# Optimization experiments

Measured on AMD Instinct MI355X. Metric: run time of the kernel, lower is better.

Reference implementation:

```python
import jax, jax.numpy as jnp
import numpy as np

OUTCOMES = [8, 8, 8, 8, 8, 8]           # concept outcome counts (concepts_order)
N_TOTAL = int(np.prod(OUTCOMES))        # 262144 joint states
N_VALID = 8192                          # admissible states
B, D = 4096, 1024


def setup_inputs() -> dict:
    key = jax.random.key(0)
    k1, k2 = jax.random.split(key)
    embeddings = jax.random.normal(k1, (B, D), dtype=jnp.float32)
    W = jax.random.normal(k2, (N_VALID, D), dtype=jnp.float32) * 0.02
    b = jnp.zeros((N_VALID,), dtype=jnp.float32)
    # unique sorted admissible-state indices, like torch.argwhere(mask)
    rng = np.random.default_rng(0)
    valid_states = jnp.asarray(
        np.sort(rng.choice(N_TOTAL, size=N_VALID, replace=False)).astype(np.int32))
    return {"embeddings": embeddings, "W": W, "b": b, "valid_states": valid_states}


def reference(embeddings, W, b, valid_states):
    # softmax over valid states: [B, N_VALID]
    probs = jax.nn.softmax(embeddings @ W.T + b, axis=1)
    probs_t = probs.T  # [N_VALID, B] for leading-axis segment reduction
    marginals = []
    stride = N_TOTAL
    for n_i in OUTCOMES:
        stride //= n_i
        # digit of each valid joint-state index along this concept's axis
        digit = (valid_states // stride) % n_i  # [N_VALID]
        # equivalent to scattering probs into the full joint tensor and
        # summing over all other concept axes, without materializing it
        m = jax.ops.segment_sum(probs_t, digit, num_segments=n_i).T  # [B, n_i]
        marginals.append(m)
    return jnp.stack(marginals)  # [n_concepts, B, 8]
```

## Files before the change

kernel.cpp:

```cpp
#include <hip/hip_runtime.h>
#include <hip/hip_bf16.h>
#include <cstdint>
#include <cstddef>

typedef __bf16 bf16_t;
typedef bf16_t bf16x8 __attribute__((ext_vector_type(8)));
typedef bf16_t bf16x4 __attribute__((ext_vector_type(4)));
typedef float  f32x4  __attribute__((ext_vector_type(4)));
typedef float  f32x16 __attribute__((ext_vector_type(16)));
typedef unsigned int u32;

#define BROWS 4096
#define NV    8192
#define KD    1024
#define NT    16
#define ST    48
#define LOG2E 1.44269504088896340736f

#define GLL(gsrc, ldst) \
  __builtin_amdgcn_global_load_lds((const __attribute__((address_space(1))) u32*)(gsrc), \
                                   (__attribute__((address_space(3))) u32*)(ldst), 16, 0, 0)
#define FENCE asm volatile("" ::: "memory")

__global__ void prep_kernel(const float* __restrict__ E, const float* __restrict__ W,
                            const int* __restrict__ vs,
                            bf16_t* __restrict__ Eb, bf16_t* __restrict__ Wb,
                            bf16_t* __restrict__ s2t) {
  const int nE = BROWS * KD / 4;
  const int nW = NV * KD / 4;
  const int nS = ST * NV / 8;
  const int nT = nE + nW + nS;
  int idx = blockIdx.x * blockDim.x + threadIdx.x;
  int stride = gridDim.x * blockDim.x;
  for (int i = idx; i < nT; i += stride) {
    if (i < nE + nW) {
      const float4* s; bf16x4* d; int j;
      if (i < nE) { s = (const float4*)E; d = (bf16x4*)Eb; j = i; }
      else        { s = (const float4*)W; d = (bf16x4*)Wb; j = i - nE; }
      float4 v = s[j];
      bf16x4 o;
      o[0] = (bf16_t)v.x; o[1] = (bf16_t)v.y; o[2] = (bf16_t)v.z; o[3] = (bf16_t)v.w;
      d[j] = o;
    } else {
      int u  = i - nE - nW;
      int b  = u >> 10;
      int i0 = (u & 1023) * 8;
      int c = b >> 3, d = b & 7, sh = 15 - 3 * c;
      bf16x8 o;
#pragma unroll
      for (int e = 0; e < 8; ++e)
        o[e] = (bf16_t)((((vs[i0 + e] >> sh) & 7) == d) ? 1.0f : 0.0f);
      *(bf16x8*)(s2t + (size_t)b * NV + i0) = o;
    }
  }
}

__global__ __launch_bounds__(512, 2)
void gemm_fused_kernel(const bf16_t* __restrict__ W, const bf16_t* __restrict__ E,
                       const float* __restrict__ bias, const bf16_t* __restrict__ s2t,
                       float* __restrict__ part) {
  __shared__ __align__(16) char lds[2][65536];
  #define AKH0 0
  #define AKH1 16384
  #define BKH0 32768
  #define BKH1 49152
  #define SOFF 75776

  const int t    = threadIdx.x;
  const int lane = t & 63;
  const int wv   = t >> 6;
  const int wm   = wv >> 2;
  const int wn   = wv & 3;
  const int fr   = lane & 15;
  const int fq   = lane >> 4;
  const int l31  = lane & 31;
  const int hi   = lane >> 5;

  int bid = blockIdx.x;
  int wg  = (bid & 7) * 64 + (bid >> 3);
  const int stile = wg >> 4;
  const int btile = wg & 15;
  const int st0 = stile * 256;
  const int bt0 = btile * 256;

  const int srow = lane >> 2;
  const int skel = ((lane & 3) ^ ((lane >> 3) & 3)) * 8;
  const bf16_t* aptr = W + (size_t)(st0 + wv * 32 + srow) * KD + skel;
  const bf16_t* bptr = E + (size_t)(bt0 + wv * 32 + srow) * KD + skel;
  const int dchunk = (wv * 2) * 1024;

  const int inner  = (hi * 16) ^ ((l31 & 6) << 3);
  const int a_base = wm * 8192 + l31 * 64 + inner;
  const int b_base = wn * 4096 + l31 * 64 + inner;

  f32x16 acc[4][2] = {};

  GLL(aptr,                &lds[0][AKH0 + dchunk]);
  GLL(aptr + 16 * KD,      &lds[0][AKH0 + dchunk + 1024]);
  GLL(bptr,                &lds[0][BKH0 + dchunk]);
  GLL(bptr + 16 * KD,      &lds[0][BKH0 + dchunk + 1024]);
  GLL(aptr + 32,           &lds[0][AKH1 + dchunk]);
  GLL(aptr + 32 + 16 * KD, &lds[0][AKH1 + dchunk + 1024]);
  GLL(bptr + 32,           &lds[0][BKH1 + dchunk]);
  GLL(bptr + 32 + 16 * KD, &lds[0][BKH1 + dchunk + 1024]);
  asm volatile("s_waitcnt vmcnt(0)" ::: "memory");
  __builtin_amdgcn_s_barrier();
  FENCE;

  int cur = 0;
  for (int kt = 0; kt < NT; ++kt) {
    const char* bufp = lds[cur];
    char* nbuf = lds[cur ^ 1];
    const bool pf = (kt + 1 < NT);

    bf16x8 a0[4][2], b0[2][2], a1[4][2], b1[2][2];

#pragma unroll
    for (int n = 0; n < 2; ++n)
#pragma unroll
      for (int ks = 0; ks < 2; ++ks)
        b0[n][ks] = *(const bf16x8*)(bufp + BKH0 + (b_base ^ (ks << 5)) + n * 2048);
#pragma unroll
    for (int m = 0; m < 4; ++m)
#pragma unroll
      for (int ks = 0; ks < 2; ++ks)
        a0[m][ks] = *(const bf16x8*)(bufp + AKH0 + (a_base ^ (ks << 5)) + m * 2048);

    if (pf) {
      const bf16_t* an = aptr + (kt + 1) * 64;
      const bf16_t* bn = bptr + (kt + 1) * 64;
      GLL(an,                &nbuf[AKH0 + dchunk]);
      GLL(an + 16 * KD,      &nbuf[AKH0 + dchunk + 1024]);
      GLL(bn,                &nbuf[BKH0 + dchunk]);
      GLL(bn + 16 * KD,      &nbuf[BKH0 + dchunk + 1024]);
      GLL(an + 32,           &nbuf[AKH1 + dchunk]);
      GLL(an + 32 + 16 * KD, &nbuf[AKH1 + dchunk + 1024]);
      GLL(bn + 32,           &nbuf[BKH1 + dchunk]);
      GLL(bn + 32 + 16 * KD, &nbuf[BKH1 + dchunk + 1024]);
    }

#pragma unroll
    for (int n = 0; n < 2; ++n)
#pragma unroll
      for (int ks = 0; ks < 2; ++ks)
        b1[n][ks] = *(const bf16x8*)(bufp + BKH1 + (b_base ^ (ks << 5)) + n * 2048);
#pragma unroll
    for (int m = 0; m < 4; ++m)
#pragma unroll
      for (int ks = 0; ks < 2; ++ks)
        a1[m][ks] = *(const bf16x8*)(bufp + AKH1 + (a_base ^ (ks << 5)) + m * 2048);

    __builtin_amdgcn_s_setprio(1);
#pragma unroll
    for (int ks = 0; ks < 2; ++ks)
#pragma unroll
      for (int m = 0; m < 4; ++m)
#pragma unroll
        for (int n = 0; n < 2; ++n)
          acc[m][n] = __builtin_amdgcn_mfma_f32_32x32x16_bf16(a0[m][ks], b0[n][ks], acc[m][n], 0, 0, 0);
#pragma unroll
    for (int ks = 0; ks < 2; ++ks)
#pragma unroll
      for (int m = 0; m < 4; ++m)
#pragma unroll
        for (int n = 0; n < 2; ++n)
          acc[m][n] = __builtin_amdgcn_mfma_f32_32x32x16_bf16(a1[m][ks], b1[n][ks], acc[m][n], 0, 0, 0);
    __builtin_amdgcn_s_setprio(0);

    asm volatile("s_waitcnt vmcnt(0)" ::: "memory");
    __builtin_amdgcn_sched_barrier(0);
    __builtin_amdgcn_s_barrier();
    FENCE;
    cur ^= 1;
  }

  char* const ldsf = &lds[0][0];

  bf16x8 sreg[3];
#pragma unroll
  for (int q = 0; q < 3; ++q) {
    const int c = t * 3 + q;
    sreg[q] = *(const bf16x8*)(s2t + (size_t)(c >> 5) * NV + st0 + (c & 31) * 8);
  }

  float* const ppart = part + (size_t)bt0 * (32 * ST) + (size_t)stile * ST;

#pragma unroll
  for (int pass = 0; pass < 2; ++pass) {
    if ((wn >> 1) == pass) {
      const int j = (wn & 1) * 64 + l31;
#pragma unroll
      for (int m = 0; m < 4; ++m)
#pragma unroll
        for (int n = 0; n < 2; ++n)
#pragma unroll
          for (int g = 0; g < 4; ++g) {
            const float4 bb = *(const float4*)&bias[st0 + wm * 128 + m * 32 + g * 8 + hi * 4];
            bf16x4 ev;
            ev[0] = (bf16_t)exp2f((acc[m][n][g * 4 + 0] + bb.x) * LOG2E);
            ev[1] = (bf16_t)exp2f((acc[m][n][g * 4 + 1] + bb.y) * LOG2E);
            ev[2] = (bf16_t)exp2f((acc[m][n][g * 4 + 2] + bb.z) * LOG2E);
            ev[3] = (bf16_t)exp2f((acc[m][n][g * 4 + 3] + bb.w) * LOG2E);
            *(bf16x4*)(ldsf + (j + n * 32) * 592 + wm * 256 + m * 64 + g * 16 + hi * 8) = ev;
          }
    }
    if (pass == 0) {
#pragma unroll
      for (int q = 0; q < 3; ++q) {
        const int c = t * 3 + q;
        *(bf16x8*)(ldsf + SOFF + (c >> 5) * 592 + (c & 31) * 16) = sreg[q];
      }
    }
    __syncthreads();

    f32x4 acc2[3] = {{0.f,0.f,0.f,0.f},{0.f,0.f,0.f,0.f},{0.f,0.f,0.f,0.f}};
#pragma unroll
    for (int k2 = 0; k2 < 8; ++k2) {
      const bf16x8 ea = *(const bf16x8*)(ldsf + (wv * 16 + fr) * 592 + k2 * 64 + fq * 16);
#pragma unroll
      for (int n2 = 0; n2 < 3; ++n2) {
        const bf16x8 sb = *(const bf16x8*)(ldsf + SOFF + (n2 * 16 + fr) * 592 + k2 * 64 + fq * 16);
        acc2[n2] = __builtin_amdgcn_mfma_f32_16x16x32_bf16(ea, sb, acc2[n2], 0, 0, 0);
      }
    }
    const int jg = pass * 128 + wv * 16 + fq * 4;
#pragma unroll
    for (int n2 = 0; n2 < 3; ++n2)
#pragma unroll
      for (int r = 0; r < 4; ++r)
        ppart[(size_t)(jg + r) * (32 * ST) + n2 * 16 + fr] = acc2[n2][r];
    __syncthreads();
  }
}

__global__ __launch_bounds__(64)
void reduce_kernel(const float* __restrict__ part, float* __restrict__ out) {
  const int b = blockIdx.x;
  const int t = threadIdx.x;
  __shared__ float fin[ST];
  if (t < ST) {
    const float* p = part + (size_t)b * (32 * ST) + t;
    float s = 0.f;
#pragma unroll
    for (int mt = 0; mt < 32; ++mt)
      s += p[mt * ST];
    fin[t] = s;
  }
  __syncthreads();
  if (t < ST) {
    float total = fin[0] + fin[1] + fin[2] + fin[3] + fin[4] + fin[5] + fin[6] + fin[7];
    out[(size_t)(t >> 3) * BROWS * 8 + (size_t)b * 8 + (t & 7)] = fin[t] / total;
  }
}

extern "C" void kernel_launch(void* const* d_in, const int* in_sizes, int n_in,
                              void* d_out, int out_size, void* d_ws, size_t ws_size,
                              hipStream_t stream) {
  const float* E    = (const float*)d_in[0];
  const float* W    = (const float*)d_in[1];
  const float* bias = (const float*)d_in[2];
  const int*   vs   = (const int*)d_in[3];
  float* out = (float*)d_out;

  char* ws = (char*)d_ws;
  size_t off = 0;
  bf16_t* Eb   = (bf16_t*)(ws + off); off += (size_t)BROWS * KD * 2;
  bf16_t* Wb   = (bf16_t*)(ws + off); off += (size_t)NV * KD * 2;
  bf16_t* s2t  = (bf16_t*)(ws + off); off += (size_t)ST * NV * 2;
  float*  part = (float*)(ws + off);  off += (size_t)BROWS * 32 * ST * 4;

  prep_kernel<<<3072, 256, 0, stream>>>(E, W, vs, Eb, Wb, s2t);
  gemm_fused_kernel<<<512, 512, 0, stream>>>(Wb, Eb, bias, s2t, part);
  reduce_kernel<<<BROWS, 64, 0, stream>>>(part, out);
}
```

Measured before the change: 109.1 us.

## Switch main GEMM to 16x16x32 MFMA tiles with XOR-swizzled LDS epilogue

Replaces the 32x32x16 MFMA accumulation with 16x16x32 MFMAs over an 8x4 accumulator grid and rewrites the LDS read addressing and swizzle to match. The epilogue now stores exp values in an XOR-swizzled 512-byte row layout instead of padded 592-byte rows. The indicator matrix is loaded straight into LDS with global_load_lds, using a pre-swizzled layout produced in the prep kernel. The aims are fewer LDS bank conflicts, no register staging for the indicator tiles, and a possibly better MFMA issue pattern. The cost is more MFMA instructions per k-step, since each one covers a smaller tile.

```diff
diff --git a/kernel.cpp b/kernel.cpp
--- a/kernel.cpp
+++ b/kernel.cpp
@@ -7,7 +7,6 @@
 typedef bf16_t bf16x8 __attribute__((ext_vector_type(8)));
 typedef bf16_t bf16x4 __attribute__((ext_vector_type(4)));
 typedef float  f32x4  __attribute__((ext_vector_type(4)));
-typedef float  f32x16 __attribute__((ext_vector_type(16)));
 typedef unsigned int u32;
 
 #define BROWS 4096
@@ -45,11 +44,12 @@
       int u  = i - nE - nW;
       int b  = u >> 10;
       int i0 = (u & 1023) * 8;
+      int base = i0 ^ ((b & 7) << 3);
       int c = b >> 3, d = b & 7, sh = 15 - 3 * c;
       bf16x8 o;
 #pragma unroll
       for (int e = 0; e < 8; ++e)
-        o[e] = (bf16_t)((((vs[i0 + e] >> sh) & 7) == d) ? 1.0f : 0.0f);
+        o[e] = (bf16_t)((((vs[base + e] >> sh) & 7) == d) ? 1.0f : 0.0f);
       *(bf16x8*)(s2t + (size_t)b * NV + i0) = o;
     }
   }
@@ -64,7 +64,6 @@
   #define AKH1 16384
   #define BKH0 32768
   #define BKH1 49152
-  #define SOFF 75776
 
   const int t    = threadIdx.x;
   const int lane = t & 63;
@@ -73,8 +72,6 @@
   const int wn   = wv & 3;
   const int fr   = lane & 15;
   const int fq   = lane >> 4;
-  const int l31  = lane & 31;
-  const int hi   = lane >> 5;
 
   int bid = blockIdx.x;
   int wg  = (bid & 7) * 64 + (bid >> 3);
@@ -89,11 +86,11 @@
   const bf16_t* bptr = E + (size_t)(bt0 + wv * 32 + srow) * KD + skel;
   const int dchunk = (wv * 2) * 1024;
 
-  const int inner  = (hi * 16) ^ ((l31 & 6) << 3);
-  const int a_base = wm * 8192 + l31 * 64 + inner;
-  const int b_base = wn * 4096 + l31 * 64 + inner;
-
-  f32x16 acc[4][2] = {};
+  const int xsw    = (fr & 6) << 3;
+  const int a_base = wm * 8192 + ((fr * 64 + fq * 16) ^ xsw);
+  const int b_base = wn * 4096 + ((fr * 64 + fq * 16) ^ xsw);
+
+  f32x4 acc[8][4] = {};
 
   GLL(aptr,                &lds[0][AKH0 + dchunk]);
   GLL(aptr + 16 * KD,      &lds[0][AKH0 + dchunk + 1024]);
@@ -113,18 +110,14 @@
     char* nbuf = lds[cur ^ 1];
     const bool pf = (kt + 1 < NT);
 
-    bf16x8 a0[4][2], b0[2][2], a1[4][2], b1[2][2];
-
-#pragma unroll
-    for (int n = 0; n < 2; ++n)
-#pragma unroll
-      for (int ks = 0; ks < 2; ++ks)
-        b0[n][ks] = *(const bf16x8*)(bufp + BKH0 + (b_base ^ (ks << 5)) + n * 2048);
-#pragma unroll
-    for (int m = 0; m < 4; ++m)
-#pragma unroll
-      for (int ks = 0; ks < 2; ++ks)
-        a0[m][ks] = *(const bf16x8*)(bufp + AKH0 + (a_base ^ (ks << 5)) + m * 2048);
+    bf16x8 a0[8], b0[4], a1[8], b1[4];
+
+#pragma unroll
+    for (int n = 0; n < 4; ++n)
+      b0[n] = *(const bf16x8*)(bufp + b_base + BKH0 + n * 1024);
+#pragma unroll
+    for (int m = 0; m < 8; ++m)
+      a0[m] = *(const bf16x8*)(bufp + a_base + AKH0 + m * 1024);
 
     if (pf) {
       const bf16_t* an = aptr + (kt + 1) * 64;
@@ -140,31 +133,23 @@
     }
 
 #pragma unroll
-    for (int n = 0; n < 2; ++n)
-#pragma unroll
-      for (int ks = 0; ks < 2; ++ks)
-        b1[n][ks] = *(const bf16x8*)(bufp + BKH1 + (b_base ^ (ks << 5)) + n * 2048);
-#pragma unroll
-    for (int m = 0; m < 4; ++m)
-#pragma unroll
-      for (int ks = 0; ks < 2; ++ks)
-        a1[m][ks] = *(const bf16x8*)(bufp + AKH1 + (a_base ^ (ks << 5)) + m * 2048);
+    for (int n = 0; n < 4; ++n)
+      b1[n] = *(const bf16x8*)(bufp + b_base + BKH1 + n * 1024);
+#pragma unroll
+    for (int m = 0; m < 8; ++m)
+      a1[m] = *(const bf16x8*)(bufp + a_base + AKH1 + m * 1024);
 
     __builtin_amdgcn_s_setprio(1);
 #pragma unroll
-    for (int ks = 0; ks < 2; ++ks)
-#pragma unroll
-      for (int m = 0; m < 4; ++m)
-#pragma unroll
-        for (int n = 0; n < 2; ++n)
-          acc[m][n] = __builtin_amdgcn_mfma_f32_32x32x16_bf16(a0[m][ks], b0[n][ks], acc[m][n], 0, 0, 0);
-#pragma unroll
-    for (int ks = 0; ks < 2; ++ks)
-#pragma unroll
-      for (int m = 0; m < 4; ++m)
-#pragma unroll
-        for (int n = 0; n < 2; ++n)
-          acc[m][n] = __builtin_amdgcn_mfma_f32_32x32x16_bf16(a1[m][ks], b1[n][ks], acc[m][n], 0, 0, 0);
+    for (int m = 0; m < 8; ++m)
+#pragma unroll
+      for (int n = 0; n < 4; ++n)
+        acc[m][n] = __builtin_amdgcn_mfma_f32_16x16x32_bf16(a0[m], b0[n], acc[m][n], 0, 0, 0);
+#pragma unroll
+    for (int m = 0; m < 8; ++m)
+#pragma unroll
+      for (int n = 0; n < 4; ++n)
+        acc[m][n] = __builtin_amdgcn_mfma_f32_16x16x32_bf16(a1[m], b1[n], acc[m][n], 0, 0, 0);
     __builtin_amdgcn_s_setprio(0);
 
     asm volatile("s_waitcnt vmcnt(0)" ::: "memory");
@@ -175,12 +160,13 @@
   }
 
   char* const ldsf = &lds[0][0];
-
-  bf16x8 sreg[3];
-#pragma unroll
-  for (int q = 0; q < 3; ++q) {
-    const int c = t * 3 + q;
-    sreg[q] = *(const bf16x8*)(s2t + (size_t)(c >> 5) * NV + st0 + (c & 31) * 8);
+  {
+#pragma unroll
+    for (int q = 0; q < 3; ++q) {
+      const bf16_t* src = s2t + (size_t)(wv * 6 + q * 2 + (lane >> 5)) * NV
+                          + st0 + (lane & 31) * 8;
+      GLL(src, ldsf + 65536 + wv * 3072 + q * 1024);
+    }
   }
 
   float* const ppart = part + (size_t)bt0 * (32 * ST) + (size_t)stile * ST;
@@ -188,38 +174,33 @@
 #pragma unroll
   for (int pass = 0; pass < 2; ++pass) {
     if ((wn >> 1) == pass) {
-      const int j = (wn & 1) * 64 + l31;
-#pragma unroll
-      for (int m = 0; m < 4; ++m)
-#pragma unroll
-        for (int n = 0; n < 2; ++n)
-#pragma unroll
-          for (int g = 0; g < 4; ++g) {
-            const float4 bb = *(const float4*)&bias[st0 + wm * 128 + m * 32 + g * 8 + hi * 4];
-            bf16x4 ev;
-            ev[0] = (bf16_t)exp2f((acc[m][n][g * 4 + 0] + bb.x) * LOG2E);
-            ev[1] = (bf16_t)exp2f((acc[m][n][g * 4 + 1] + bb.y) * LOG2E);
-            ev[2] = (bf16_t)exp2f((acc[m][n][g * 4 + 2] + bb.z) * LOG2E);
-            ev[3] = (bf16_t)exp2f((acc[m][n][g * 4 + 3] + bb.w) * LOG2E);
-            *(bf16x4*)(ldsf + (j + n * 32) * 592 + wm * 256 + m * 64 + g * 16 + hi * 8) = ev;
-          }
-    }
-    if (pass == 0) {
-#pragma unroll
-      for (int q = 0; q < 3; ++q) {
-        const int c = t * 3 + q;
-        *(bf16x8*)(ldsf + SOFF + (c >> 5) * 592 + (c & 31) * 16) = sreg[q];
+#pragma unroll
+      for (int m = 0; m < 8; ++m) {
+        const float4 bb = *(const float4*)&bias[st0 + wm * 128 + m * 16 + fq * 4];
+#pragma unroll
+        for (int n = 0; n < 4; ++n) {
+          bf16x4 ev;
+          ev[0] = (bf16_t)exp2f((acc[m][n][0] + bb.x) * LOG2E);
+          ev[1] = (bf16_t)exp2f((acc[m][n][1] + bb.y) * LOG2E);
+          ev[2] = (bf16_t)exp2f((acc[m][n][2] + bb.z) * LOG2E);
+          ev[3] = (bf16_t)exp2f((acc[m][n][3] + bb.w) * LOG2E);
+          const int jh = (wn & 1) * 64 + n * 16 + fr;
+          const int ib = (wm * 128 + m * 16 + fq * 4) * 2;
+          *(bf16x4*)(ldsf + jh * 512 + (ib ^ ((fr & 7) << 4))) = ev;
+        }
       }
     }
+    if (pass == 0) asm volatile("s_waitcnt vmcnt(0)" ::: "memory");
     __syncthreads();
 
     f32x4 acc2[3] = {{0.f,0.f,0.f,0.f},{0.f,0.f,0.f,0.f},{0.f,0.f,0.f,0.f}};
 #pragma unroll
     for (int k2 = 0; k2 < 8; ++k2) {
-      const bf16x8 ea = *(const bf16x8*)(ldsf + (wv * 16 + fr) * 592 + k2 * 64 + fq * 16);
+      const int ko2 = (k2 * 64 + fq * 16) ^ ((fr & 7) << 4);
+      const bf16x8 ea = *(const bf16x8*)(ldsf + (wv * 16 + fr) * 512 + ko2);
 #pragma unroll
       for (int n2 = 0; n2 < 3; ++n2) {
-        const bf16x8 sb = *(const bf16x8*)(ldsf + SOFF + (n2 * 16 + fr) * 592 + k2 * 64 + fq * 16);
+        const bf16x8 sb = *(const bf16x8*)(ldsf + 65536 + (n2 * 16 + fr) * 512 + ko2);
         acc2[n2] = __builtin_amdgcn_mfma_f32_16x16x32_bf16(ea, sb, acc2[n2], 0, 0, 0);
       }
     }
```

Measured after the change: 99.30 us. 9.0% less time.
